# Optimization experiments

Hardware: AMD Instinct MI355X
Metric: run time of the kernel (lower is better)

## Reference

```python
import jax, jax.numpy as jnp
import numpy as np

B, N, S, K = 16, 4096, 1024, 32
DIN, DINC, DOUT = 64, 67, 64
MAX_VALUE = 1e10


def setup_inputs() -> dict:
    key = jax.random.key(0)
    ks = jax.random.split(key, 6)
    x = jax.random.normal(ks[0], (B, N, DIN), dtype=jnp.float32)
    x_complete = jax.random.normal(ks[1], (B, N, DINC), dtype=jnp.float32)
    # neighbor indices in [-1, N); -1 denotes padding (masked out in pooling)
    indexes = jax.random.randint(ks[2], (B, S, K), -1, N, dtype=jnp.int64)
    # first neighbor is the center point and must be valid
    indexes = indexes.at[:, :, 0].set(jnp.abs(indexes[:, :, 0]) % N)
    weight1 = jax.random.normal(ks[3], (DOUT, DINC), dtype=jnp.float32) * 0.05
    weight2 = jax.random.normal(ks[4], (DOUT, DIN), dtype=jnp.float32) * 0.05
    bias = jax.random.normal(ks[5], (DOUT,), dtype=jnp.float32) * 0.05
    return {"x": x, "x_complete": x_complete, "indexes": indexes,
            "weight1": weight1, "weight2": weight2, "bias": bias, "use_x": 1}


def reference(x, x_complete, indexes, weight1, weight2, bias, use_x):
    # pooling_operation = 'max' (hardcoded; string arg in original module)
    Bq, Nq, _ = x.shape
    _, Sq, Kq = indexes.shape
    C = weight1.shape[0]
    # dense linear projections
    xc = jnp.einsum('bnd,cd->bnc', x_complete, weight1) + bias  # (B,N,C)
    xp = jnp.einsum('bnd,cd->bnc', x, weight2)                  # (B,N,C)
    if use_x:
        xc = xc + xp
    # prepend a zero row so index -1 (-> slot 0) gathers zeros
    pad = jnp.concatenate([jnp.zeros((Bq, 1, C), xc.dtype), xc], axis=1)  # (B,N+1,C)
    idx1 = indexes + 1                                          # (B,S,K)
    g = jnp.take_along_axis(pad, idx1.reshape(Bq, Sq * Kq, 1), axis=1)
    g = g.reshape(Bq, Sq, Kq, C)                                # (B,S,K,C)
    if use_x:
        if Nq == Sq:
            g = g - xp[:, :, None, :]
        else:
            xp_pad = jnp.concatenate([jnp.zeros((Bq, 1, C), xp.dtype), xp], axis=1)
            center = jnp.take_along_axis(xp_pad, (indexes[:, :, 0] + 1)[:, :, None], axis=1)  # (B,S,C)
            g = g - center[:, :, None, :]
    # masked max over the neighbor axis: padded slots pushed to -MAX_VALUE
    mask = (idx1 == 0).astype(g.dtype)[..., None]               # (B,S,K,1)
    out = jnp.max(g - MAX_VALUE * mask, axis=2)                 # (B,S,C)
    return out
```

## Files before the change

### kernel.cpp

```cpp
#include <hip/hip_runtime.h>

#define B_    16
#define N_    4096
#define S_    1024
#define K_    32
#define DIN_  64
#define DINC_ 67
#define DOUT_ 64
#define ROWS_ (B_ * N_)
#define NCH   128
#define NTILE 28
#define NFRAG (NTILE * 64)
#define ASTR  168
#define WLDSB (NTILE * 64 * 16)
#define ALDSB (64 * ASTR * 2)

typedef float f32x4 __attribute__((ext_vector_type(4)));
typedef short s16x8 __attribute__((ext_vector_type(8)));

static __device__ __forceinline__ unsigned short f2bf(float f) {
    unsigned int u = __float_as_uint(f);
    u = (u + 0x7fffu + ((u >> 16) & 1u)) >> 16;
    return (unsigned short)u;
}
static __device__ __forceinline__ float bf2f(unsigned short h) {
    return __uint_as_float((unsigned int)h << 16);
}
static __device__ __forceinline__ unsigned int pack2(float a, float b) {
    return (unsigned int)f2bf(a) | ((unsigned int)f2bf(b) << 16);
}

__global__ __launch_bounds__(256) void prep_kernel(
    const float* __restrict__ w1, const float* __restrict__ w2,
    const int* __restrict__ use_x_p, uint4* __restrict__ wf)
{
    const int id = blockIdx.x * 256 + threadIdx.x;
    if (id >= NFRAG) return;
    const int tile = id >> 6;
    const int l    = id & 63;
    const int s    = (tile < 16) ? (tile >> 3) : (2 + ((tile - 16) >> 2));
    const int nt   = (tile < 16) ? (tile & 7)  : ((tile - 16) & 3);
    const int q    = l >> 4, m = l & 15;
    const int c    = nt * 16 + m;
    const int ux   = use_x_p[0];

    unsigned int w[4];
#pragma unroll
    for (int p = 0; p < 4; ++p) {
        unsigned short h[2];
#pragma unroll
        for (int e = 0; e < 2; ++e) {
            const int k = s * 32 + q * 8 + p * 2 + e;
            float v = 0.f;
            if (c < 64) {
                if (k < 64)         v = ux ? w2[c * DIN_ + k] : 0.f;
                else if (k < 131)   v = w1[c * DINC_ + (k - 64)];
            } else {
                if (k < 64)         v = w2[(c - 64) * DIN_ + k];
            }
            h[e] = f2bf(v);
        }
        w[p] = (unsigned int)h[0] | ((unsigned int)h[1] << 16);
    }
    wf[id] = make_uint4(w[0], w[1], w[2], w[3]);
}

__global__ __launch_bounds__(256) void proj_kernel(
    const float* __restrict__ x, const float* __restrict__ xcm,
    const uint4* __restrict__ wf, const float* __restrict__ bias,
    unsigned short* __restrict__ cmb)
{
    __shared__ char smem[WLDSB + ALDSB];
    uint4* ldsb          = (uint4*)smem;
    unsigned short* lact = (unsigned short*)(smem + WLDSB);
    unsigned int*  ldsd  = (unsigned int*)lact;

    const int t    = threadIdx.x;
    const int row0 = (blockIdx.x & 7) * (ROWS_ / 8) + (blockIdx.x >> 3) * 64;

#pragma unroll
    for (int j = 0; j < 7; ++j) {
        const int idx = j * 256 + t;
        __builtin_amdgcn_global_load_lds(
            (const __attribute__((address_space(1))) void*)(wf + idx),
            (__attribute__((address_space(3))) void*)(ldsb + idx), 16, 0, 0);
    }

    {
        const float4* sx4 = (const float4*)(x + (size_t)row0 * DIN_);
#pragma unroll
        for (int j = 0; j < 4; ++j) {
            const int idx = j * 256 + t;
            const float4 v = sx4[idx];
            const int row = idx >> 4, f4 = idx & 15;
            *(uint2*)(ldsd + row * 84 + f4 * 2) =
                make_uint2(pack2(v.x, v.y), pack2(v.z, v.w));
        }
    }
    {
        const float4* sc4 = (const float4*)(xcm + (size_t)row0 * DINC_);
#pragma unroll
        for (int j = 0; j < 5; ++j) {
            const int idx = j * 256 + t;
            if (j < 4 || idx < 1072) {
                const float4 v = sc4[idx];
                const float e4[4] = {v.x, v.y, v.z, v.w};
#pragma unroll
                for (int e = 0; e < 4; ++e) {
                    const int ee  = 4 * idx + e;
                    const int row = ee / 67;
                    const int d   = ee - row * 67;
                    lact[row * ASTR + 64 + d] = f2bf(e4[e]);
                }
            }
        }
    }
    if (t < 64) lact[t * ASTR + 131] = 0;
    for (int i = t; i < 64 * 14; i += 256) {
        const int row = i / 14, j2 = i - row * 14;
        ldsd[row * 84 + 66 + j2] = 0;
    }
    __syncthreads();

    const int l = t & 63;
    const int w = __builtin_amdgcn_readfirstlane(t >> 6);
    const int q = l >> 4, m = l & 15;

    const unsigned short* arow = lact + (w * 16 + m) * ASTR;
    s16x8 af[5];
#pragma unroll
    for (int s = 0; s < 5; ++s)
        af[s] = *(const s16x8*)(arow + s * 32 + q * 8);

    const s16x8* bfr = (const s16x8*)ldsb;

    f32x4 acc[8];
#pragma unroll
    for (int nt = 0; nt < 8; ++nt) acc[nt] = (f32x4){0.f, 0.f, 0.f, 0.f};

#pragma unroll
    for (int s = 0; s < 2; ++s)
#pragma unroll
        for (int nt = 0; nt < 8; ++nt)
            acc[nt] = __builtin_amdgcn_mfma_f32_16x16x32_bf16(
                bfr[(s * 8 + nt) * 64 + l], af[s], acc[nt], 0, 0, 0);
#pragma unroll
    for (int s = 2; s < 5; ++s)
#pragma unroll
        for (int nt = 0; nt < 4; ++nt)
            acc[nt] = __builtin_amdgcn_mfma_f32_16x16x32_bf16(
                bfr[(16 + (s - 2) * 4 + nt) * 64 + l], af[s], acc[nt], 0, 0, 0);

    const int row_g = row0 + w * 16 + m;
    unsigned short* rowp = cmb + (size_t)row_g * NCH;
    const int chq = q * 4;
#pragma unroll
    for (int nt = 0; nt < 8; ++nt) {
        f32x4 a = acc[nt];
        if (nt < 4) {
            const float4 bv = *(const float4*)(bias + nt * 16 + chq);
            a[0] += bv.x; a[1] += bv.y; a[2] += bv.z; a[3] += bv.w;
        }
        *(uint2*)(rowp + nt * 16 + chq) =
            make_uint2(pack2(a[0], a[1]), pack2(a[2], a[3]));
    }
}

__global__ __launch_bounds__(256) void gather_max_kernel(
    const int* __restrict__ indexes, const unsigned short* __restrict__ cmb,
    const int* __restrict__ use_x_p, float* __restrict__ out)
{
    const int lane = threadIdx.x & 63;
    const int h    = lane >> 5;
    const int ln   = lane & 31;
    const int wv   = __builtin_amdgcn_readfirstlane(threadIdx.x >> 6);
    const int grp  = (blockIdx.x & 7) * 1024 + (blockIdx.x >> 3) * 4 + wv;
    const int pairA = grp * 2;
    const int b     = grp >> 9;
    const int ux    = use_x_p[0];

    const int* iA = indexes + (size_t)pairA * K_;
    const int* iB = iA + K_;
    const char* cb = (const char*)cmb + (size_t)b * N_ * 256;

    const float NEG = -__builtin_inff();
    float m0 = NEG, m1 = NEG;
#pragma unroll
    for (int k = 0; k < K_; ++k) {
        const int ia = iA[k], ib = iB[k];
        const int ik = h ? ib : ia;
        const int iku = ik < 0 ? 0 : ik;
        const unsigned int v = *(const unsigned int*)(cb + ((size_t)iku << 8) + ln * 4);
        const bool inv = ik < 0;
        m0 = fmaxf(m0, inv ? NEG : bf2f((unsigned short)(v & 0xffff)));
        m1 = fmaxf(m1, inv ? NEG : bf2f((unsigned short)(v >> 16)));
    }
    if (ux) {
        const int i0 = h ? iB[0] : iA[0];
        const unsigned int c = *(const unsigned int*)(cb + ((size_t)i0 << 8) + 128 + ln * 4);
        m0 -= bf2f((unsigned short)(c & 0xffff));
        m1 -= bf2f((unsigned short)(c >> 16));
    }
    const int pair = pairA + h;
    *(float2*)(out + (size_t)pair * 64 + ln * 2) = make_float2(m0, m1);
}

__global__ __launch_bounds__(256, 1) void fused_fallback_kernel(
    const float* __restrict__ x, const float* __restrict__ xcm,
    const int* __restrict__ indexes,
    const float* __restrict__ w1, const float* __restrict__ w2,
    const float* __restrict__ bias, const int* __restrict__ use_x_p,
    float* __restrict__ out)
{
    const int lane = threadIdx.x & 63;
    const int pair = (blockIdx.x * blockDim.x + threadIdx.x) >> 6;
    const int b    = pair >> 10;
    const int ux   = use_x_p[0];

    float W1[DINC_];
#pragma unroll
    for (int j = 0; j < DINC_; ++j) W1[j] = w1[lane * DINC_ + j];
    float W2[DIN_];
#pragma unroll
    for (int j = 0; j < DIN_; ++j) W2[j] = w2[lane * DIN_ + j];
    const float bv = bias[lane];

    const int* idxp  = indexes + (size_t)pair * K_;
    const int  myidx = idxp[lane & 31];

    const float NEG = -__builtin_inff();
    float m = NEG;
    for (int k = 0; k < K_; ++k) {
        const int ik = __shfl(myidx, k, 64);
        if (ik < 0) continue;
        const float* xc_row = xcm + ((size_t)b * N_ + ik) * DINC_;
        float a1 = bv;
#pragma unroll
        for (int j = 0; j < DINC_; ++j) a1 += xc_row[j] * W1[j];
        if (ux) {
            const float* x_row = x + ((size_t)b * N_ + ik) * DIN_;
            float a2 = 0.f;
#pragma unroll
            for (int j = 0; j < DIN_; ++j) a2 += x_row[j] * W2[j];
            a1 += a2;
        }
        m = fmaxf(m, a1);
    }
    if (ux) {
        const int i0 = __shfl(myidx, 0, 64);
        const float* x_row = x + ((size_t)b * N_ + i0) * DIN_;
        float a2 = 0.f;
#pragma unroll
        for (int j = 0; j < DIN_; ++j) a2 += x_row[j] * W2[j];
        m -= a2;
    }
    out[(size_t)pair * DOUT_ + lane] = m;
}

extern "C" void kernel_launch(void* const* d_in, const int* in_sizes, int n_in,
                              void* d_out, int out_size, void* d_ws, size_t ws_size,
                              hipStream_t stream)
{
    const float* x    = (const float*)d_in[0];
    const float* xcm  = (const float*)d_in[1];
    const int*   idx  = (const int*)d_in[2];
    const float* w1   = (const float*)d_in[3];
    const float* w2   = (const float*)d_in[4];
    const float* bias = (const float*)d_in[5];
    const int*   ux   = (const int*)d_in[6];
    float* out = (float*)d_out;

    const size_t cmb_bytes = (size_t)ROWS_ * NCH * sizeof(unsigned short);
    const size_t wf_bytes  = (size_t)NFRAG * 16;
    const int npairs = B_ * S_;

    if (ws_size >= cmb_bytes + wf_bytes) {
        unsigned short* cmb = (unsigned short*)d_ws;
        uint4* wf = (uint4*)((char*)d_ws + cmb_bytes);

        prep_kernel<<<(NFRAG + 255) / 256, 256, 0, stream>>>(w1, w2, ux, wf);
        proj_kernel<<<ROWS_ / 64, 256, 0, stream>>>(x, xcm, wf, bias, cmb);
        gather_max_kernel<<<(npairs / 2) / 4, 256, 0, stream>>>(idx, cmb, ux, out);
    } else {
        fused_fallback_kernel<<<npairs / 4, 256, 0, stream>>>(x, xcm, idx, w1, w2,
                                                              bias, ux, out);
    }
}
```

Measured before the change: 104.6 us.

## Fuse projection and gather-max into one persistent kernel with per-batch-group grid barrier

Merges the projection and gather-max kernels into one 512-block kernel. Each block projects two 64-row tiles, then waits on an atomic counter shared by the 64 blocks of its batch group before doing the masked gather-max for its pairs. prep_kernel now also zeroes the barrier counters. This removes one kernel launch and the gap between kernels, and lets each group start gathering once its own rows are written. The cost is a spin-wait barrier that assumes all 64 blocks of a group are resident at the same time, which risks deadlock if they are not, and fewer blocks in flight to hide latency.

```diff
diff --git a/kernel.cpp b/kernel.cpp
--- a/kernel.cpp
+++ b/kernel.cpp
@@ -14,6 +14,7 @@
 #define ASTR  168
 #define WLDSB (NTILE * 64 * 16)
 #define ALDSB (64 * ASTR * 2)
+#define NBLK  512
 
 typedef float f32x4 __attribute__((ext_vector_type(4)));
 typedef short s16x8 __attribute__((ext_vector_type(8)));
@@ -32,10 +33,15 @@
 
 __global__ __launch_bounds__(256) void prep_kernel(
     const float* __restrict__ w1, const float* __restrict__ w2,
-    const int* __restrict__ use_x_p, uint4* __restrict__ wf)
+    const int* __restrict__ use_x_p, uint4* __restrict__ wf,
+    unsigned int* __restrict__ bar)
 {
     const int id = blockIdx.x * 256 + threadIdx.x;
-    if (id >= NFRAG) return;
+    if (id >= NFRAG) {
+        const int z = id - NFRAG;
+        if (z < 128) bar[z] = 0u;
+        return;
+    }
     const int tile = id >> 6;
     const int l    = id & 63;
     const int s    = (tile < 16) ? (tile >> 3) : (2 + ((tile - 16) >> 2));
@@ -65,18 +71,22 @@
     wf[id] = make_uint4(w[0], w[1], w[2], w[3]);
 }
 
-__global__ __launch_bounds__(256) void proj_kernel(
+__global__ __launch_bounds__(256, 2) void fused_kernel(
     const float* __restrict__ x, const float* __restrict__ xcm,
     const uint4* __restrict__ wf, const float* __restrict__ bias,
-    unsigned short* __restrict__ cmb)
+    const int* __restrict__ indexes, const int* __restrict__ use_x_p,
+    unsigned short* __restrict__ cmb, unsigned int* __restrict__ bar,
+    float* __restrict__ out)
 {
     __shared__ char smem[WLDSB + ALDSB];
     uint4* ldsb          = (uint4*)smem;
     unsigned short* lact = (unsigned short*)(smem + WLDSB);
     unsigned int*  ldsd  = (unsigned int*)lact;
 
-    const int t    = threadIdx.x;
-    const int row0 = (blockIdx.x & 7) * (ROWS_ / 8) + (blockIdx.x >> 3) * 64;
+    const int t  = threadIdx.x;
+    const int g  = blockIdx.x & 7;
+    const int bs = blockIdx.x >> 3;
+    const int ux = use_x_p[0];
 
 #pragma unroll
     for (int j = 0; j < 7; ++j) {
@@ -86,123 +96,138 @@
             (__attribute__((address_space(3))) void*)(ldsb + idx), 16, 0, 0);
     }
 
-    {
-        const float4* sx4 = (const float4*)(x + (size_t)row0 * DIN_);
-#pragma unroll
-        for (int j = 0; j < 4; ++j) {
-            const int idx = j * 256 + t;
-            const float4 v = sx4[idx];
-            const int row = idx >> 4, f4 = idx & 15;
-            *(uint2*)(ldsd + row * 84 + f4 * 2) =
-                make_uint2(pack2(v.x, v.y), pack2(v.z, v.w));
-        }
-    }
-    {
-        const float4* sc4 = (const float4*)(xcm + (size_t)row0 * DINC_);
-#pragma unroll
-        for (int j = 0; j < 5; ++j) {
-            const int idx = j * 256 + t;
-            if (j < 4 || idx < 1072) {
-                const float4 v = sc4[idx];
-                const float e4[4] = {v.x, v.y, v.z, v.w};
-#pragma unroll
-                for (int e = 0; e < 4; ++e) {
-                    const int ee  = 4 * idx + e;
-                    const int row = ee / 67;
-                    const int d   = ee - row * 67;
-                    lact[row * ASTR + 64 + d] = f2bf(e4[e]);
-                }
-            }
-        }
-    }
-    if (t < 64) lact[t * ASTR + 131] = 0;
-    for (int i = t; i < 64 * 14; i += 256) {
-        const int row = i / 14, j2 = i - row * 14;
-        ldsd[row * 84 + 66 + j2] = 0;
-    }
-    __syncthreads();
-
     const int l = t & 63;
     const int w = __builtin_amdgcn_readfirstlane(t >> 6);
     const int q = l >> 4, m = l & 15;
 
-    const unsigned short* arow = lact + (w * 16 + m) * ASTR;
-    s16x8 af[5];
-#pragma unroll
-    for (int s = 0; s < 5; ++s)
-        af[s] = *(const s16x8*)(arow + s * 32 + q * 8);
-
-    const s16x8* bfr = (const s16x8*)ldsb;
-
-    f32x4 acc[8];
-#pragma unroll
-    for (int nt = 0; nt < 8; ++nt) acc[nt] = (f32x4){0.f, 0.f, 0.f, 0.f};
-
-#pragma unroll
-    for (int s = 0; s < 2; ++s)
-#pragma unroll
-        for (int nt = 0; nt < 8; ++nt)
-            acc[nt] = __builtin_amdgcn_mfma_f32_16x16x32_bf16(
-                bfr[(s * 8 + nt) * 64 + l], af[s], acc[nt], 0, 0, 0);
-#pragma unroll
-    for (int s = 2; s < 5; ++s)
-#pragma unroll
-        for (int nt = 0; nt < 4; ++nt)
-            acc[nt] = __builtin_amdgcn_mfma_f32_16x16x32_bf16(
-                bfr[(16 + (s - 2) * 4 + nt) * 64 + l], af[s], acc[nt], 0, 0, 0);
-
-    const int row_g = row0 + w * 16 + m;
-    unsigned short* rowp = cmb + (size_t)row_g * NCH;
-    const int chq = q * 4;
-#pragma unroll
-    for (int nt = 0; nt < 8; ++nt) {
-        f32x4 a = acc[nt];
-        if (nt < 4) {
-            const float4 bv = *(const float4*)(bias + nt * 16 + chq);
-            a[0] += bv.x; a[1] += bv.y; a[2] += bv.z; a[3] += bv.w;
-        }
-        *(uint2*)(rowp + nt * 16 + chq) =
-            make_uint2(pack2(a[0], a[1]), pack2(a[2], a[3]));
-    }
-}
-
-__global__ __launch_bounds__(256) void gather_max_kernel(
-    const int* __restrict__ indexes, const unsigned short* __restrict__ cmb,
-    const int* __restrict__ use_x_p, float* __restrict__ out)
-{
-    const int lane = threadIdx.x & 63;
-    const int h    = lane >> 5;
-    const int ln   = lane & 31;
-    const int wv   = __builtin_amdgcn_readfirstlane(threadIdx.x >> 6);
-    const int grp  = (blockIdx.x & 7) * 1024 + (blockIdx.x >> 3) * 4 + wv;
-    const int pairA = grp * 2;
-    const int b     = grp >> 9;
-    const int ux    = use_x_p[0];
-
-    const int* iA = indexes + (size_t)pairA * K_;
-    const int* iB = iA + K_;
-    const char* cb = (const char*)cmb + (size_t)b * N_ * 256;
-
+#pragma unroll 1
+    for (int it = 0; it < 2; ++it) {
+        const int row0 = g * (ROWS_ / 8) + (bs * 2 + it) * 64;
+
+        {
+            const float4* sx4 = (const float4*)(x + (size_t)row0 * DIN_);
+#pragma unroll
+            for (int j = 0; j < 4; ++j) {
+                const int idx = j * 256 + t;
+                const float4 v = sx4[idx];
+                const int row = idx >> 4, f4 = idx & 15;
+                *(uint2*)(ldsd + row * 84 + f4 * 2) =
+                    make_uint2(pack2(v.x, v.y), pack2(v.z, v.w));
+            }
+        }
+        {
+            const float4* sc4 = (const float4*)(xcm + (size_t)row0 * DINC_);
+#pragma unroll
+            for (int j = 0; j < 5; ++j) {
+                const int idx = j * 256 + t;
+                if (j < 4 || idx < 1072) {
+                    const float4 v = sc4[idx];
+                    const float e4[4] = {v.x, v.y, v.z, v.w};
+#pragma unroll
+                    for (int e = 0; e < 4; ++e) {
+                        const int ee  = 4 * idx + e;
+                        const int row = ee / 67;
+                        const int d   = ee - row * 67;
+                        lact[row * ASTR + 64 + d] = f2bf(e4[e]);
+                    }
+                }
+            }
+        }
+        if (t < 64) lact[t * ASTR + 131] = 0;
+        for (int i = t; i < 64 * 14; i += 256) {
+            const int row = i / 14, j2 = i - row * 14;
+            ldsd[row * 84 + 66 + j2] = 0;
+        }
+        __syncthreads();
+
+        const unsigned short* arow = lact + (w * 16 + m) * ASTR;
+        s16x8 af[5];
+#pragma unroll
+        for (int s = 0; s < 5; ++s)
+            af[s] = *(const s16x8*)(arow + s * 32 + q * 8);
+
+        const s16x8* bfr = (const s16x8*)ldsb;
+
+        f32x4 acc[8];
+#pragma unroll
+        for (int nt = 0; nt < 8; ++nt) acc[nt] = (f32x4){0.f, 0.f, 0.f, 0.f};
+
+#pragma unroll
+        for (int s = 0; s < 2; ++s)
+#pragma unroll
+            for (int nt = 0; nt < 8; ++nt)
+                acc[nt] = __builtin_amdgcn_mfma_f32_16x16x32_bf16(
+                    bfr[(s * 8 + nt) * 64 + l], af[s], acc[nt], 0, 0, 0);
+#pragma unroll
+        for (int s = 2; s < 5; ++s)
+#pragma unroll
+            for (int nt = 0; nt < 4; ++nt)
+                acc[nt] = __builtin_amdgcn_mfma_f32_16x16x32_bf16(
+                    bfr[(16 + (s - 2) * 4 + nt) * 64 + l], af[s], acc[nt], 0, 0, 0);
+
+        const int row_g = row0 + w * 16 + m;
+        unsigned short* rowp = cmb + (size_t)row_g * NCH;
+        const int chq = q * 4;
+#pragma unroll
+        for (int nt = 0; nt < 8; ++nt) {
+            f32x4 a = acc[nt];
+            if (nt < 4) {
+                const float4 bv = *(const float4*)(bias + nt * 16 + chq);
+                a[0] += bv.x; a[1] += bv.y; a[2] += bv.z; a[3] += bv.w;
+            }
+            *(uint2*)(rowp + nt * 16 + chq) =
+                make_uint2(pack2(a[0], a[1]), pack2(a[2], a[3]));
+        }
+        __syncthreads();
+    }
+
+    __threadfence();
+    __syncthreads();
+    if (t == 0) {
+        __hip_atomic_fetch_add(&bar[g * 16], 1u, __ATOMIC_RELEASE,
+                               __HIP_MEMORY_SCOPE_AGENT);
+        while (__hip_atomic_load(&bar[g * 16], __ATOMIC_ACQUIRE,
+                                 __HIP_MEMORY_SCOPE_AGENT) < 64u)
+            __builtin_amdgcn_s_sleep(2);
+    }
+    __syncthreads();
+
+    const int h  = l >> 5;
+    const int ln = l & 31;
     const float NEG = -__builtin_inff();
-    float m0 = NEG, m1 = NEG;
-#pragma unroll
-    for (int k = 0; k < K_; ++k) {
-        const int ia = iA[k], ib = iB[k];
-        const int ik = h ? ib : ia;
-        const int iku = ik < 0 ? 0 : ik;
-        const unsigned int v = *(const unsigned int*)(cb + ((size_t)iku << 8) + ln * 4);
-        const bool inv = ik < 0;
-        m0 = fmaxf(m0, inv ? NEG : bf2f((unsigned short)(v & 0xffff)));
-        m1 = fmaxf(m1, inv ? NEG : bf2f((unsigned short)(v >> 16)));
-    }
-    if (ux) {
-        const int i0 = h ? iB[0] : iA[0];
-        const unsigned int c = *(const unsigned int*)(cb + ((size_t)i0 << 8) + 128 + ln * 4);
-        m0 -= bf2f((unsigned short)(c & 0xffff));
-        m1 -= bf2f((unsigned short)(c >> 16));
-    }
-    const int pair = pairA + h;
-    *(float2*)(out + (size_t)pair * 64 + ln * 2) = make_float2(m0, m1);
+
+#pragma unroll 1
+    for (int gi = 0; gi < 4; ++gi) {
+        const int grp   = g * 1024 + bs * 16 + w * 4 + gi;
+        const int pairA = grp * 2;
+        const int b     = grp >> 9;
+
+        const int* iA = indexes + (size_t)pairA * K_;
+        const int* iB = iA + K_;
+        const char* cb = (const char*)cmb + (size_t)b * N_ * 256;
+
+        float m0 = NEG, m1 = NEG;
+#pragma unroll
+        for (int k = 0; k < K_; ++k) {
+            const int ia = iA[k], ib = iB[k];
+            const int ik = h ? ib : ia;
+            const int iku = ik < 0 ? 0 : ik;
+            const unsigned int v =
+                *(const unsigned int*)(cb + ((size_t)iku << 8) + ln * 4);
+            const bool inv = ik < 0;
+            m0 = fmaxf(m0, inv ? NEG : bf2f((unsigned short)(v & 0xffff)));
+            m1 = fmaxf(m1, inv ? NEG : bf2f((unsigned short)(v >> 16)));
+        }
+        if (ux) {
+            const int i0 = h ? iB[0] : iA[0];
+            const unsigned int c =
+                *(const unsigned int*)(cb + ((size_t)i0 << 8) + 128 + ln * 4);
+            m0 -= bf2f((unsigned short)(c & 0xffff));
+            m1 -= bf2f((unsigned short)(c >> 16));
+        }
+        const int pair = pairA + h;
+        *(float2*)(out + (size_t)pair * 64 + ln * 2) = make_float2(m0, m1);
+    }
 }
 
 __global__ __launch_bounds__(256, 1) void fused_fallback_kernel(
@@ -272,15 +297,17 @@
 
     const size_t cmb_bytes = (size_t)ROWS_ * NCH * sizeof(unsigned short);
     const size_t wf_bytes  = (size_t)NFRAG * 16;
+    const size_t bar_bytes = 128 * sizeof(unsigned int);
     const int npairs = B_ * S_;
 
-    if (ws_size >= cmb_bytes + wf_bytes) {
+    if (ws_size >= cmb_bytes + wf_bytes + bar_bytes) {
         unsigned short* cmb = (unsigned short*)d_ws;
         uint4* wf = (uint4*)((char*)d_ws + cmb_bytes);
-
-        prep_kernel<<<(NFRAG + 255) / 256, 256, 0, stream>>>(w1, w2, ux, wf);
-        proj_kernel<<<ROWS_ / 64, 256, 0, stream>>>(x, xcm, wf, bias, cmb);
-        gather_max_kernel<<<(npairs / 2) / 4, 256, 0, stream>>>(idx, cmb, ux, out);
+        unsigned int* bar = (unsigned int*)((char*)d_ws + cmb_bytes + wf_bytes);
+
+        prep_kernel<<<8, 256, 0, stream>>>(w1, w2, ux, wf, bar);
+        fused_kernel<<<NBLK, 256, 0, stream>>>(x, xcm, wf, bias, idx, ux,
+                                               cmb, bar, out);
     } else {
         fused_fallback_kernel<<<npairs / 4, 256, 0, stream>>>(x, xcm, idx, w1, w2,
                                                               bias, ux, out);
```

Result: slower. 191.4 us (+82.9%).
